# Kernel tuning notes

Measured on AMD Instinct MI355X. Metric: run time of the kernel, lower is better.

## Reference

```python
import jax, jax.numpy as jnp
import numpy as np

B, C, T = 64, 8, 2048
K, DIL = 64, 1
NF = 32                      # n_frequencies (<= K//2+1 = 33)
MLP, HID = 32, 64
FFT_DIM = C * NF * 2         # 512
W = T - DIL * (K - 1)        # 1985 windows (== max_windows)


def setup_inputs() -> dict:
    key = jax.random.key(0)
    ks = jax.random.split(key, 12)
    s = 0.05
    return {
        "x": jax.random.normal(ks[0], (B, C, T), jnp.float32),
        "proj_w": jax.random.normal(ks[1], (MLP, FFT_DIM), jnp.float32) * s,
        "proj_b": jax.random.normal(ks[2], (MLP,), jnp.float32) * s,
        "w0": jax.random.normal(ks[3], (HID, MLP), jnp.float32) * s,      # Linear(32->64)
        "b0": jax.random.normal(ks[4], (HID,), jnp.float32) * s,
        "a0": jnp.ones((HID,), jnp.float32),                              # Snake a (a_init=1)
        "w1": jax.random.normal(ks[5], (MLP, HID), jnp.float32) * s,      # Linear(64->32)
        "b1": jax.random.normal(ks[6], (MLP,), jnp.float32) * s,
        "a1": jnp.ones((MLP,), jnp.float32),
        "wo": jax.random.normal(ks[7], (1, MLP), jnp.float32) * s,        # output Linear(32->1)
        "bo": jax.random.normal(ks[8], (1,), jnp.float32) * s,
        "agg": jax.random.normal(ks[9], (W,), jnp.float32) * s,           # agg_weights
    }


def _snake(x, a):
    aa = jnp.abs(a) + 1e-8
    return x + jnp.sin(aa * x) ** 2 / aa


def reference(x, proj_w, proj_b, w0, b0, a0, w1, b1, a1, wo, bo, agg):
    eff = DIL * (K - 1)
    # window t uses sorted indices t-(K-1)*DIL, ..., t  (step DIL)
    idx = eff + jnp.arange(W)[:, None] - (K - 1 - jnp.arange(K))[None, :] * DIL  # [W,K]
    win = x[:, :, idx]                                   # [B,C,W,K]
    fft = jnp.fft.rfft(win, axis=-1)[..., :NF]           # [B,C,W,NF] complex
    mag = jnp.log1p(jnp.abs(fft))
    ph = jnp.arctan2(fft.imag, fft.real) / np.pi
    feat = jnp.stack([mag, ph], axis=-1)                 # [B,C,W,NF,2]
    feat = jnp.transpose(feat, (0, 2, 1, 3, 4)).reshape(B, W, FFT_DIM)
    proj = jnp.tanh(feat @ proj_w.T + proj_b) * np.pi    # [B,W,MLP]
    h = _snake(proj @ w0.T + b0, a0)                     # [B,W,HID]
    h = _snake(h @ w1.T + b1, a1)                        # [B,W,MLP]
    out_t = (h @ wo.T + bo)[..., 0]                      # [B,W]
    wts = jax.nn.softmax(agg)                            # [W]
    return jnp.sum(out_t * wts, axis=1)                  # [B]
```

## Files before the change

kernel.cpp:

```cpp
#include <hip/hip_runtime.h>
#include <math.h>

#define B_ 64
#define C_ 8
#define T_ 2048
#define NF_ 32
#define MLP_ 32
#define HID_ 64
#define W_ 1985
#define CH_ 32
#define NCHUNK_ 63
#define PI_F 3.14159265358979323846f

typedef _Float16 f16x8 __attribute__((ext_vector_type(8)));
typedef _Float16 f16x2 __attribute__((ext_vector_type(2)));
typedef float    f32x4 __attribute__((ext_vector_type(4)));

#define WS_PARTIAL 64
#define WS_TWHI    4096
#define WS_TWLO    6144
#define WS_PWPK    8192

__device__ __forceinline__ float fast_rcp(float x) { return __builtin_amdgcn_rcpf(x); }

__device__ __forceinline__ float fast_atan2pi(float y, float x)
{
    const float ax = fabsf(x), ay = fabsf(y);
    const float mx = fmaxf(ax, ay), mn = fminf(ax, ay);
    const float r  = mn * fast_rcp(fmaxf(mx, 1e-30f));
    const float t  = r * r;
    float a = -0.003730950f;
    a = fmaf(a, t,  0.016759940f);
    a = fmaf(a, t, -0.037059946f);
    a = fmaf(a, t,  0.061602941f);
    a = fmaf(a, t, -0.105877528f);
    a = fmaf(a, t,  0.318302656f);
    a *= r;
    a = (ay > ax) ? (0.5f - a) : a;
    a = (x < 0.0f) ? (1.0f - a) : a;
    return copysignf(a, y);
}

__device__ __forceinline__ float fast_tanh(float x)
{
    const float e = __expf(2.0f * x);
    return 1.0f - 2.0f * fast_rcp(e + 1.0f);
}

__device__ __forceinline__ float fast_snake(float h, float rcp_aa, float aa)
{
    const float s = __sinf(aa * h);
    return h + s * s * rcp_aa;
}

__device__ __forceinline__ float dot4(float4 a, float4 b, float acc)
{
    return fmaf(a.x, b.x, fmaf(a.y, b.y, fmaf(a.z, b.z, fmaf(a.w, b.w, acc))));
}

__device__ __forceinline__ unsigned packhl(float v)
{
    const _Float16 h = (_Float16)v;
    const _Float16 l = (_Float16)(v - (float)h);
    f16x2 p; p[0] = h; p[1] = l;
    return __builtin_bit_cast(unsigned, p);
}

__device__ __forceinline__ void unpack8(const unsigned* u, f16x8& ah, f16x8& al)
{
    union { unsigned w[4]; f16x8 v; } H, L;
    #pragma unroll
    for (int j = 0; j < 4; ++j) {
        H.w[j] = __builtin_amdgcn_perm(u[2*j+1], u[2*j], 0x05040100u);
        L.w[j] = __builtin_amdgcn_perm(u[2*j+1], u[2*j], 0x07060302u);
    }
    ah = H.v; al = L.v;
}

__device__ __forceinline__ void gload_lds16(const void* g, void* l)
{
    __builtin_amdgcn_global_load_lds(
        (const __attribute__((address_space(1))) void*)g,
        (__attribute__((address_space(3))) void*)l, 16, 0, 0);
}

__global__ __launch_bounds__(1024) void k_pre(
    const float* __restrict__ agg, const float* __restrict__ pw,
    float* __restrict__ ws)
{
    __shared__ float red[1024];
    const int t = threadIdx.x;

    _Float16* twHi = (_Float16*)(ws + WS_TWHI);
    _Float16* twLo = (_Float16*)(ws + WS_TWLO);
    #pragma unroll
    for (int e = 0; e < 4; ++e) {
        const int id = t * 4 + e;
        const int n = id >> 6, k = id & 63;
        const int f = n & 31;
        float s, c;
        sincosf(0.0981747704246810387f * (float)((k * f) & 63), &s, &c);
        const float v = (n < 32) ? c : -s;
        const _Float16 h = (_Float16)v;
        twHi[id] = h;
        twLo[id] = (_Float16)(v - (float)h);
    }

    unsigned* pwpk = (unsigned*)(ws + WS_PWPK);
    #pragma unroll
    for (int e = 0; e < 16; ++e) {
        const int id = e * 1024 + t;
        pwpk[id] = packhl(pw[id]);
    }

    float m = -1e30f;
    for (int i = t; i < W_; i += 1024) m = fmaxf(m, agg[i]);
    red[t] = m;
    __syncthreads();
    for (int s = 512; s > 0; s >>= 1) {
        if (t < s) red[t] = fmaxf(red[t], red[t + s]);
        __syncthreads();
    }
    const float mx = red[0];
    __syncthreads();
    float sum = 0.f;
    for (int i = t; i < W_; i += 1024) sum += __expf(agg[i] - mx);
    red[t] = sum;
    __syncthreads();
    for (int s = 512; s > 0; s >>= 1) {
        if (t < s) red[t] += red[t + s];
        __syncthreads();
    }
    if (t == 0) { ws[0] = mx; ws[1] = red[0]; }
}

__global__ __launch_bounds__(1024, 8) void k_main(
    const float* __restrict__ x,  const float* __restrict__ pw,
    const float* __restrict__ pb, const float* __restrict__ w0g,
    const float* __restrict__ b0g,const float* __restrict__ a0g,
    const float* __restrict__ w1g,const float* __restrict__ b1g,
    const float* __restrict__ a1g,const float* __restrict__ wog,
    const float* __restrict__ bog,const float* __restrict__ agg,
    const float* __restrict__ wsp, float* __restrict__ partial)
{
    __shared__ __align__(16) _Float16 twHiL[64 * 64];
    __shared__ __align__(16) _Float16 twLoL[64 * 64];
    __shared__ __align__(16) unsigned featH[32 * 256];
    __shared__ __align__(16) unsigned xtileP[C_][100];
    __shared__ __align__(16) float w0L[64 * 36];
    __shared__ __align__(16) float w1L[32 * 68];
    __shared__ __align__(16) float projL[32 * 36];
    __shared__ float smalls[260];
    __shared__ float chunkAcc[CH_];

    float* pacc = (float*)featH;
    float* h0L  = (float*)featH;
    float* h1L  = (float*)featH + 2176;

    const int t     = threadIdx.x;
    const int chunk = blockIdx.x;
    const int b     = blockIdx.y;
    const int w0c   = chunk * CH_;
    const int wid   = t >> 6;
    const int lane  = t & 63;
    const int m16   = lane & 15;
    const int kl    = lane >> 4;
    const int cdft  = wid >> 1;

    {
        const int gl = (wid & 7) * 64 + lane;
        const int n  = gl >> 3, q = gl & 7;
        const int srcg = n * 8 + (q ^ (n & 7));
        const float* srcbase = wsp + ((wid < 8) ? WS_TWHI : WS_TWLO);
        _Float16* dst = ((wid < 8) ? twHiL : twLoL) + gl * 8;
        gload_lds16((const char*)srcbase + srcg * 16, dst);
    }

    if (t < C_ * 96) {
        const int c = t / 96;
        const int j = t - c * 96;
        int gi = w0c + j; if (gi > T_ - 1) gi = T_ - 1;
        xtileP[c][j] = packhl(x[((size_t)b * C_ + c) * T_ + gi]);
    }
    if (t < 257) {
        float smv;
        if      (t <  32) smv = pb[t];
        else if (t <  96) smv = b0g[t - 32];
        else if (t < 160) smv = a0g[t - 96];
        else if (t < 192) smv = b1g[t - 160];
        else if (t < 224) smv = a1g[t - 192];
        else if (t < 256) smv = wog[t - 224];
        else              smv = bog[0];
        smalls[t] = smv;
    }
    if (t < 512) {
        const float4 w0r = ((const float4*)w0g)[t];
        const int o0 = t >> 3, k40 = t & 7;
        *(float4*)&w0L[o0 * 36 + k40 * 4] = w0r;
    } else {
        const int u = t - 512;
        const float4 w1r = ((const float4*)w1g)[u];
        const int o1 = u >> 4, k41 = u & 15;
        *(float4*)&w1L[o1 * 68 + k41 * 4] = w1r;
    }
    __syncthreads();

    f32x4 dacc0 = {0.f,0.f,0.f,0.f}, dacc1 = {0.f,0.f,0.f,0.f};
    f32x4 dacc2 = {0.f,0.f,0.f,0.f}, dacc3 = {0.f,0.f,0.f,0.f};
    const int wra = (wid & 1) * 16 + m16;
    {
        #pragma unroll
        for (int kstep = 0; kstep < 2; ++kstep) {
            const int kq = kstep * 4 + kl;
            unsigned ut[8];
            #pragma unroll
            for (int j = 0; j < 8; ++j) ut[j] = xtileP[cdft][wra + kq * 8 + j];
            f16x8 ah, al; unpack8(ut, ah, al);
            f32x4* dp[4] = { &dacc0, &dacc1, &dacc2, &dacc3 };
            #pragma unroll
            for (int nt = 0; nt < 4; ++nt) {
                const int nrow = nt * 16 + m16;
                const int gB = (nrow * 8 + (kq ^ (nrow & 7))) * 8;
                const f16x8 bh = *(const f16x8*)&twHiL[gB];
                const f16x8 bl = *(const f16x8*)&twLoL[gB];
                f32x4 a = *dp[nt];
                a = __builtin_amdgcn_mfma_f32_16x16x32_f16(ah, bh, a, 0, 0, 0);
                a = __builtin_amdgcn_mfma_f32_16x16x32_f16(al, bh, a, 0, 0, 0);
                a = __builtin_amdgcn_mfma_f32_16x16x32_f16(ah, bl, a, 0, 0, 0);
                *dp[nt] = a;
            }
        }
    }

    unsigned heldM[2][4], heldP[2][4];
    {
        const int wbase = (wid & 1) * 16 + kl * 4;
        const int ccl   = cdft & 3;
        const float reA[2][4] = {{dacc0[0],dacc0[1],dacc0[2],dacc0[3]},
                                 {dacc1[0],dacc1[1],dacc1[2],dacc1[3]}};
        const float imA[2][4] = {{dacc2[0],dacc2[1],dacc2[2],dacc2[3]},
                                 {dacc3[0],dacc3[1],dacc3[2],dacc3[3]}};
        #pragma unroll
        for (int fi = 0; fi < 2; ++fi) {
            const int f = fi * 16 + m16;
            #pragma unroll
            for (int r = 0; r < 4; ++r) {
                const int w  = wbase + r;
                const float re = reA[fi][r], im = imA[fi][r];
                const float mag = __logf(1.0f + __builtin_amdgcn_sqrtf(re*re + im*im));
                const float ph  = fast_atan2pi(im, re);
                const unsigned um = packhl(mag), up = packhl(ph);
                if (wid < 8) {
                    const int g  = ccl * 16 + fi * 8 + (m16 >> 1);
                    const int gs = g ^ (w & 7);
                    *(uint2*)&featH[w * 256 + gs * 4 + 2 * (f & 1)] =
                        make_uint2(um, up);
                } else {
                    heldM[fi][r] = um; heldP[fi][r] = up;
                }
            }
        }
    }
    __syncthreads();

    const unsigned* pwpk = (const unsigned*)(wsp + WS_PWPK);
    {
        const int wt = (wid >> 1) & 1;
        const int ot = wid & 1;
        const int kq4 = wid >> 2;
        const int arow = wt * 16 + m16;
        const int brow = ot * 16 + m16;
        f32x4 acc = {0.f, 0.f, 0.f, 0.f};
        #pragma unroll
        for (int p = 0; p < 2; ++p) {
            #pragma unroll
            for (int kstep = 0; kstep < 2; ++kstep) {
                const int kp = kq4 * 64 + kstep * 32 + kl * 8;
                const unsigned* bp = pwpk + (size_t)brow * 512 + p * 256 + kp;
                unsigned ub[8];
                *(uint4*)&ub[0] = *(const uint4*)bp;
                *(uint4*)&ub[4] = *(const uint4*)(bp + 4);
                f16x8 bh, bl; unpack8(ub, bh, bl);
                const int g0 = kp >> 2;
                unsigned ua[8];
                *(uint4*)&ua[0] = *(const uint4*)&featH[arow * 256 + ((g0    ) ^ (arow & 7)) * 4];
                *(uint4*)&ua[4] = *(const uint4*)&featH[arow * 256 + ((g0 + 1) ^ (arow & 7)) * 4];
                f16x8 ah, al; unpack8(ua, ah, al);
                acc = __builtin_amdgcn_mfma_f32_16x16x32_f16(ah, bh, acc, 0, 0, 0);
                acc = __builtin_amdgcn_mfma_f32_16x16x32_f16(al, bh, acc, 0, 0, 0);
                acc = __builtin_amdgcn_mfma_f32_16x16x32_f16(ah, bl, acc, 0, 0, 0);
            }
            if (p == 0) {
                __syncthreads();
                if (wid >= 8) {
                    const int wbase = (wid & 1) * 16 + kl * 4;
                    const int ccl   = cdft & 3;
                    #pragma unroll
                    for (int fi = 0; fi < 2; ++fi) {
                        const int f = fi * 16 + m16;
                        #pragma unroll
                        for (int r = 0; r < 4; ++r) {
                            const int w  = wbase + r;
                            const int g  = ccl * 16 + fi * 8 + (m16 >> 1);
                            const int gs = g ^ (w & 7);
                            *(uint2*)&featH[w * 256 + gs * 4 + 2 * (f & 1)] =
                                make_uint2(heldM[fi][r], heldP[fi][r]);
                        }
                    }
                }
                __syncthreads();
            }
        }
        __syncthreads();
        #pragma unroll
        for (int r = 0; r < 4; ++r) {
            const int w = wt * 16 + kl * 4 + r;
            const int o = ot * 16 + m16;
            pacc[kq4 * 1056 + w * 33 + o] = acc[r];
        }
    }
    __syncthreads();

    {
        const int o = t & 31;
        const int w = t >> 5;
        float s = smalls[o];
        #pragma unroll
        for (int q = 0; q < 4; ++q) s += pacc[q * 1056 + w * 33 + o];
        projL[w * 36 + o] = fast_tanh(s) * PI_F;
    }
    __syncthreads();

    {
        const int w = t >> 5;
        const int o = t & 31;
        float4 pr[8];
        #pragma unroll
        for (int q = 0; q < 8; ++q) pr[q] = *(const float4*)&projL[w * 36 + q * 4];
        #pragma unroll
        for (int k = 0; k < 2; ++k) {
            const int oo = o + 32 * k;
            float acc = 0.f;
            #pragma unroll
            for (int q = 0; q < 8; ++q)
                acc = dot4(pr[q], *(const float4*)&w0L[oo * 36 + q * 4], acc);
            const float hv = acc + smalls[32 + oo];
            const float aa = fabsf(smalls[96 + oo]) + 1e-8f;
            h0L[w * 68 + oo] = fast_snake(hv, fast_rcp(aa), aa);
        }
    }
    __syncthreads();

    {
        const int w = t >> 5;
        const int o = t & 31;
        float acc = 0.f;
        #pragma unroll 4
        for (int q = 0; q < 16; ++q)
            acc = dot4(*(const float4*)&h0L[w * 68 + q * 4],
                       *(const float4*)&w1L[o * 68 + q * 4], acc);
        const float hv = acc + smalls[160 + o];
        const float aa = fabsf(smalls[192 + o]) + 1e-8f;
        h1L[w * 36 + o] = fast_snake(hv, fast_rcp(aa), aa);
    }
    __syncthreads();

    if (t < CH_) {
        const int w = t;
        float acc = 0.f;
        #pragma unroll
        for (int q = 0; q < 8; ++q)
            acc = dot4(*(const float4*)&h1L[w * 36 + q * 4],
                       *(const float4*)&smalls[224 + q * 4], acc);
        const float val = acc + smalls[256];
        const int wg = w0c + w;
        const float sw = (wg < W_) ? __expf(agg[wg] - wsp[0]) / wsp[1] : 0.f;
        chunkAcc[w] = val * sw;
    }
    __syncthreads();

    if (t < 32) {
        float vs = chunkAcc[t];
        vs += __shfl_down(vs, 16);
        vs += __shfl_down(vs, 8);
        vs += __shfl_down(vs, 4);
        vs += __shfl_down(vs, 2);
        vs += __shfl_down(vs, 1);
        if (t == 0) partial[(size_t)chunk * B_ + b] = vs;
    }
}

__global__ void k_reduce(const float* __restrict__ partial, float* __restrict__ out)
{
    const int b = threadIdx.x;
    if (b < B_) {
        float s = 0.f;
        for (int c = 0; c < NCHUNK_; ++c) s += partial[(size_t)c * B_ + b];
        out[b] = s;
    }
}

extern "C" void kernel_launch(void* const* d_in, const int* in_sizes, int n_in,
                              void* d_out, int out_size, void* d_ws, size_t ws_size,
                              hipStream_t stream)
{
    const float* x   = (const float*)d_in[0];
    const float* pw  = (const float*)d_in[1];
    const float* pb  = (const float*)d_in[2];
    const float* w0  = (const float*)d_in[3];
    const float* b0  = (const float*)d_in[4];
    const float* a0  = (const float*)d_in[5];
    const float* w1  = (const float*)d_in[6];
    const float* b1  = (const float*)d_in[7];
    const float* a1  = (const float*)d_in[8];
    const float* wo  = (const float*)d_in[9];
    const float* bo  = (const float*)d_in[10];
    const float* agg = (const float*)d_in[11];
    float* ws  = (float*)d_ws;
    float* out = (float*)d_out;

    k_pre<<<1, 1024, 0, stream>>>(agg, pw, ws);
    dim3 grid(NCHUNK_, B_);
    k_main<<<grid, 1024, 0, stream>>>(x, pw, pb, w0, b0, a0, w1, b1, a1, wo, bo,
                                      agg, ws, ws + WS_PARTIAL);
    k_reduce<<<1, 64, 0, stream>>>(ws + WS_PARTIAL, out);
}
```

Baseline: 132.6 us.

## Move MLP layers to split-fp16 MFMA and store features as separate hi/lo planes

The two small MLP layers (32->64 and 64->32), previously scalar fp32 dot4 loops, now run on MFMA 16x16x32 f16 instructions using a hi/lo split (three MFMAs per step) to keep near-fp32 accuracy. Weights w0/w1 and proj_w are pre-split into separate hi and lo fp16 arrays in k_pre. Features and activations are stored in LDS as separate hi/lo planes, so the packed-word unpack (perm) step before each MFMA is gone. The aim is less ALU and LDS traffic in the per-chunk MLP stage. In exchange, only 8 and then 4 waves do the MLP work, and there is extra global traffic for the unpacked weight planes.

```diff
diff --git a/kernel.cpp b/kernel.cpp
--- a/kernel.cpp
+++ b/kernel.cpp
@@ -19,7 +19,12 @@
 #define WS_PARTIAL 64
 #define WS_TWHI    4096
 #define WS_TWLO    6144
-#define WS_PWPK    8192
+#define WS_PWHI    8192
+#define WS_PWLO    16384
+#define WS_W0HI    24576
+#define WS_W0LO    25600
+#define WS_W1HI    26624
+#define WS_W1LO    27648
 
 __device__ __forceinline__ float fast_rcp(float x) { return __builtin_amdgcn_rcpf(x); }
 
@@ -86,6 +91,7 @@
 
 __global__ __launch_bounds__(1024) void k_pre(
     const float* __restrict__ agg, const float* __restrict__ pw,
+    const float* __restrict__ w0g, const float* __restrict__ w1g,
     float* __restrict__ ws)
 {
     __shared__ float red[1024];
@@ -106,11 +112,32 @@
         twLo[id] = (_Float16)(v - (float)h);
     }
 
-    unsigned* pwpk = (unsigned*)(ws + WS_PWPK);
+    _Float16* pwHi = (_Float16*)(ws + WS_PWHI);
+    _Float16* pwLo = (_Float16*)(ws + WS_PWLO);
     #pragma unroll
     for (int e = 0; e < 16; ++e) {
         const int id = e * 1024 + t;
-        pwpk[id] = packhl(pw[id]);
+        const float v = pw[id];
+        const _Float16 h = (_Float16)v;
+        pwHi[id] = h;
+        pwLo[id] = (_Float16)(v - (float)h);
+    }
+
+    _Float16* w0Hi = (_Float16*)(ws + WS_W0HI);
+    _Float16* w0Lo = (_Float16*)(ws + WS_W0LO);
+    _Float16* w1Hi = (_Float16*)(ws + WS_W1HI);
+    _Float16* w1Lo = (_Float16*)(ws + WS_W1LO);
+    #pragma unroll
+    for (int e = 0; e < 2; ++e) {
+        const int id = e * 1024 + t;
+        const float v0 = w0g[id];
+        const _Float16 h0 = (_Float16)v0;
+        w0Hi[id] = h0;
+        w0Lo[id] = (_Float16)(v0 - (float)h0);
+        const float v1 = w1g[id];
+        const _Float16 h1 = (_Float16)v1;
+        w1Hi[id] = h1;
+        w1Lo[id] = (_Float16)(v1 - (float)h1);
     }
 
     float m = -1e30f;
@@ -143,19 +170,23 @@
     const float* __restrict__ bog,const float* __restrict__ agg,
     const float* __restrict__ wsp, float* __restrict__ partial)
 {
-    __shared__ __align__(16) _Float16 twHiL[64 * 64];
-    __shared__ __align__(16) _Float16 twLoL[64 * 64];
-    __shared__ __align__(16) unsigned featH[32 * 256];
+    __shared__ __align__(16) _Float16 twHiL[4096];
+    __shared__ __align__(16) _Float16 twLoL[4096];
+    __shared__ __align__(16) _Float16 featP[16384];
+    __shared__ __align__(16) _Float16 projP[2560];
+    __shared__ __align__(16) _Float16 h0P[4608];
     __shared__ __align__(16) unsigned xtileP[C_][100];
-    __shared__ __align__(16) float w0L[64 * 36];
-    __shared__ __align__(16) float w1L[32 * 68];
-    __shared__ __align__(16) float projL[32 * 36];
     __shared__ float smalls[260];
     __shared__ float chunkAcc[CH_];
 
-    float* pacc = (float*)featH;
-    float* h0L  = (float*)featH;
-    float* h1L  = (float*)featH + 2176;
+    _Float16* featHi = featP;
+    _Float16* featLo = featP + 8192;
+    _Float16* projHi = projP;
+    _Float16* projLo = projP + 1280;
+    _Float16* h0Hi   = h0P;
+    _Float16* h0Lo   = h0P + 2304;
+    float* pacc = (float*)featP;
+    float* h1L  = (float*)featP;
 
     const int t     = threadIdx.x;
     const int chunk = blockIdx.x;
@@ -192,16 +223,6 @@
         else if (t < 256) smv = wog[t - 224];
         else              smv = bog[0];
         smalls[t] = smv;
-    }
-    if (t < 512) {
-        const float4 w0r = ((const float4*)w0g)[t];
-        const int o0 = t >> 3, k40 = t & 7;
-        *(float4*)&w0L[o0 * 36 + k40 * 4] = w0r;
-    } else {
-        const int u = t - 512;
-        const float4 w1r = ((const float4*)w1g)[u];
-        const int o1 = u >> 4, k41 = u & 15;
-        *(float4*)&w1L[o1 * 68 + k41 * 4] = w1r;
     }
     __syncthreads();
 
@@ -232,7 +253,7 @@
         }
     }
 
-    unsigned heldM[2][4], heldP[2][4];
+    unsigned heldHi[2][4], heldLo[2][4];
     {
         const int wbase = (wid & 1) * 16 + kl * 4;
         const int ccl   = cdft & 3;
@@ -243,27 +264,35 @@
         #pragma unroll
         for (int fi = 0; fi < 2; ++fi) {
             const int f = fi * 16 + m16;
+            const int g = ccl * 8 + (f >> 2);
+            const int sub = 2 * (f & 3);
             #pragma unroll
             for (int r = 0; r < 4; ++r) {
                 const int w  = wbase + r;
                 const float re = reA[fi][r], im = imA[fi][r];
                 const float mag = __logf(1.0f + __builtin_amdgcn_sqrtf(re*re + im*im));
                 const float ph  = fast_atan2pi(im, re);
-                const unsigned um = packhl(mag), up = packhl(ph);
+                const _Float16 mh = (_Float16)mag;
+                const _Float16 qh = (_Float16)ph;
+                f16x2 vh; vh[0] = mh; vh[1] = qh;
+                f16x2 vl;
+                vl[0] = (_Float16)(mag - (float)mh);
+                vl[1] = (_Float16)(ph  - (float)qh);
                 if (wid < 8) {
-                    const int g  = ccl * 16 + fi * 8 + (m16 >> 1);
-                    const int gs = g ^ (w & 7);
-                    *(uint2*)&featH[w * 256 + gs * 4 + 2 * (f & 1)] =
-                        make_uint2(um, up);
+                    const int off = w * 256 + ((g ^ (w & 7)) * 8) + sub;
+                    *(f16x2*)&featHi[off] = vh;
+                    *(f16x2*)&featLo[off] = vl;
                 } else {
-                    heldM[fi][r] = um; heldP[fi][r] = up;
+                    heldHi[fi][r] = __builtin_bit_cast(unsigned, vh);
+                    heldLo[fi][r] = __builtin_bit_cast(unsigned, vl);
                 }
             }
         }
     }
     __syncthreads();
 
-    const unsigned* pwpk = (const unsigned*)(wsp + WS_PWPK);
+    const _Float16* pwHi = (const _Float16*)(wsp + WS_PWHI);
+    const _Float16* pwLo = (const _Float16*)(wsp + WS_PWLO);
     {
         const int wt = (wid >> 1) & 1;
         const int ot = wid & 1;
@@ -276,16 +305,12 @@
             #pragma unroll
             for (int kstep = 0; kstep < 2; ++kstep) {
                 const int kp = kq4 * 64 + kstep * 32 + kl * 8;
-                const unsigned* bp = pwpk + (size_t)brow * 512 + p * 256 + kp;
-                unsigned ub[8];
-                *(uint4*)&ub[0] = *(const uint4*)bp;
-                *(uint4*)&ub[4] = *(const uint4*)(bp + 4);
-                f16x8 bh, bl; unpack8(ub, bh, bl);
-                const int g0 = kp >> 2;
-                unsigned ua[8];
-                *(uint4*)&ua[0] = *(const uint4*)&featH[arow * 256 + ((g0    ) ^ (arow & 7)) * 4];
-                *(uint4*)&ua[4] = *(const uint4*)&featH[arow * 256 + ((g0 + 1) ^ (arow & 7)) * 4];
-                f16x8 ah, al; unpack8(ua, ah, al);
+                const f16x8 bh = *(const f16x8*)&pwHi[(size_t)brow * 512 + p * 256 + kp];
+                const f16x8 bl = *(const f16x8*)&pwLo[(size_t)brow * 512 + p * 256 + kp];
+                const int g0 = kp >> 3;
+                const int offA = arow * 256 + ((g0 ^ (arow & 7)) * 8);
+                const f16x8 ah = *(const f16x8*)&featHi[offA];
+                const f16x8 al = *(const f16x8*)&featLo[offA];
                 acc = __builtin_amdgcn_mfma_f32_16x16x32_f16(ah, bh, acc, 0, 0, 0);
                 acc = __builtin_amdgcn_mfma_f32_16x16x32_f16(al, bh, acc, 0, 0, 0);
                 acc = __builtin_amdgcn_mfma_f32_16x16x32_f16(ah, bl, acc, 0, 0, 0);
@@ -298,13 +323,14 @@
                     #pragma unroll
                     for (int fi = 0; fi < 2; ++fi) {
                         const int f = fi * 16 + m16;
+                        const int g = ccl * 8 + (f >> 2);
+                        const int sub = 2 * (f & 3);
                         #pragma unroll
                         for (int r = 0; r < 4; ++r) {
                             const int w  = wbase + r;
-                            const int g  = ccl * 16 + fi * 8 + (m16 >> 1);
-                            const int gs = g ^ (w & 7);
-                            *(uint2*)&featH[w * 256 + gs * 4 + 2 * (f & 1)] =
-                                make_uint2(heldM[fi][r], heldP[fi][r]);
+                            const int off = w * 256 + ((g ^ (w & 7)) * 8) + sub;
+                            *(unsigned*)&featHi[off] = heldHi[fi][r];
+                            *(unsigned*)&featLo[off] = heldLo[fi][r];
                         }
                     }
                 }
@@ -327,41 +353,70 @@
         float s = smalls[o];
         #pragma unroll
         for (int q = 0; q < 4; ++q) s += pacc[q * 1056 + w * 33 + o];
-        projL[w * 36 + o] = fast_tanh(s) * PI_F;
-    }
-    __syncthreads();
-
-    {
-        const int w = t >> 5;
-        const int o = t & 31;
-        float4 pr[8];
-        #pragma unroll
-        for (int q = 0; q < 8; ++q) pr[q] = *(const float4*)&projL[w * 36 + q * 4];
-        #pragma unroll
-        for (int k = 0; k < 2; ++k) {
-            const int oo = o + 32 * k;
-            float acc = 0.f;
-            #pragma unroll
-            for (int q = 0; q < 8; ++q)
-                acc = dot4(pr[q], *(const float4*)&w0L[oo * 36 + q * 4], acc);
-            const float hv = acc + smalls[32 + oo];
-            const float aa = fabsf(smalls[96 + oo]) + 1e-8f;
-            h0L[w * 68 + oo] = fast_snake(hv, fast_rcp(aa), aa);
-        }
-    }
-    __syncthreads();
-
-    {
-        const int w = t >> 5;
-        const int o = t & 31;
-        float acc = 0.f;
-        #pragma unroll 4
-        for (int q = 0; q < 16; ++q)
-            acc = dot4(*(const float4*)&h0L[w * 68 + q * 4],
-                       *(const float4*)&w1L[o * 68 + q * 4], acc);
-        const float hv = acc + smalls[160 + o];
-        const float aa = fabsf(smalls[192 + o]) + 1e-8f;
-        h1L[w * 36 + o] = fast_snake(hv, fast_rcp(aa), aa);
+        const float pr = fast_tanh(s) * PI_F;
+        const _Float16 h = (_Float16)pr;
+        projHi[w * 40 + o] = h;
+        projLo[w * 40 + o] = (_Float16)(pr - (float)h);
+    }
+    __syncthreads();
+
+    const _Float16* w0Hi = (const _Float16*)(wsp + WS_W0HI);
+    const _Float16* w0Lo = (const _Float16*)(wsp + WS_W0LO);
+    if (wid < 8) {
+        const int wt = wid & 1;
+        const int ot = wid >> 1;
+        const int arow = wt * 16 + m16;
+        const int brow = ot * 16 + m16;
+        const f16x8 ah = *(const f16x8*)&projHi[arow * 40 + kl * 8];
+        const f16x8 al = *(const f16x8*)&projLo[arow * 40 + kl * 8];
+        const f16x8 bh = *(const f16x8*)&w0Hi[brow * 32 + kl * 8];
+        const f16x8 bl = *(const f16x8*)&w0Lo[brow * 32 + kl * 8];
+        f32x4 acc = {0.f, 0.f, 0.f, 0.f};
+        acc = __builtin_amdgcn_mfma_f32_16x16x32_f16(ah, bh, acc, 0, 0, 0);
+        acc = __builtin_amdgcn_mfma_f32_16x16x32_f16(al, bh, acc, 0, 0, 0);
+        acc = __builtin_amdgcn_mfma_f32_16x16x32_f16(ah, bl, acc, 0, 0, 0);
+        const int o  = ot * 16 + m16;
+        const float b0v = smalls[32 + o];
+        const float aa  = fabsf(smalls[96 + o]) + 1e-8f;
+        const float ra  = fast_rcp(aa);
+        #pragma unroll
+        for (int r = 0; r < 4; ++r) {
+            const int w = wt * 16 + kl * 4 + r;
+            const float hv = fast_snake(acc[r] + b0v, ra, aa);
+            const _Float16 h = (_Float16)hv;
+            h0Hi[w * 72 + o] = h;
+            h0Lo[w * 72 + o] = (_Float16)(hv - (float)h);
+        }
+    }
+    __syncthreads();
+
+    const _Float16* w1Hi = (const _Float16*)(wsp + WS_W1HI);
+    const _Float16* w1Lo = (const _Float16*)(wsp + WS_W1LO);
+    if (wid < 4) {
+        const int wt = wid & 1;
+        const int ot = wid >> 1;
+        const int arow = wt * 16 + m16;
+        const int brow = ot * 16 + m16;
+        f32x4 acc = {0.f, 0.f, 0.f, 0.f};
+        #pragma unroll
+        for (int ks = 0; ks < 2; ++ks) {
+            const f16x8 ah = *(const f16x8*)&h0Hi[arow * 72 + ks * 32 + kl * 8];
+            const f16x8 al = *(const f16x8*)&h0Lo[arow * 72 + ks * 32 + kl * 8];
+            const f16x8 bh = *(const f16x8*)&w1Hi[brow * 64 + ks * 32 + kl * 8];
+            const f16x8 bl = *(const f16x8*)&w1Lo[brow * 64 + ks * 32 + kl * 8];
+            acc = __builtin_amdgcn_mfma_f32_16x16x32_f16(ah, bh, acc, 0, 0, 0);
+            acc = __builtin_amdgcn_mfma_f32_16x16x32_f16(al, bh, acc, 0, 0, 0);
+            acc = __builtin_amdgcn_mfma_f32_16x16x32_f16(ah, bl, acc, 0, 0, 0);
+        }
+        const int o  = ot * 16 + m16;
+        const float b1v = smalls[160 + o];
+        const float aa  = fabsf(smalls[192 + o]) + 1e-8f;
+        const float ra  = fast_rcp(aa);
+        #pragma unroll
+        for (int r = 0; r < 4; ++r) {
+            const int w = wt * 16 + kl * 4 + r;
+            h1L[w * 36 + o] = fast_snake(acc[r] + b1v, ra, aa);
+        }
     }
     __syncthreads();
 
@@ -419,7 +474,7 @@
     float* ws  = (float*)d_ws;
     float* out = (float*)d_out;
 
-    k_pre<<<1, 1024, 0, stream>>>(agg, pw, ws);
+    k_pre<<<1, 1024, 0, stream>>>(agg, pw, w0, w1, ws);
     dim3 grid(NCHUNK_, B_);
     k_main<<<grid, 1024, 0, stream>>>(x, pw, pb, w0, b0, a0, w1, b1, a1, wo, bo,
                                       agg, ws, ws + WS_PARTIAL);
```

Result: faster. 122.6 us (-7.6%).
